# Kernel tuning notes

Hardware: AMD Instinct MI355X
Metric: run time of the kernel (lower is better)

The kernel has to match this reference:

```python
import jax, jax.numpy as jnp
import numpy as np

EPS = 1e-5
LN_EPS = 1e-5
NUM_EXPERTS = 8
TOP_K = 2
HIDDEN = 1024
INTER = 2048


def _swiglu(x, wg, wu, wd):
    # x: [T,H]; wg,wu: [H,I]; wd: [I,H]
    return (jax.nn.silu(x @ wg) * (x @ wu)) @ wd


def setup_inputs() -> dict:
    key = jax.random.key(0)
    ks = jax.random.split(key, 10)
    B, S, H, I, E = 8, 4096, HIDDEN, INTER, NUM_EXPERTS
    std_h = 1.0 / np.sqrt(H)
    std_i = 1.0 / np.sqrt(I)
    return {
        "x": jax.random.normal(ks[0], (B, S, H), dtype=jnp.float32),
        "ln_scale": jnp.ones((H,), dtype=jnp.float32),
        "ln_bias": jnp.zeros((H,), dtype=jnp.float32),
        "gate_w": jax.random.normal(ks[1], (E, H), dtype=jnp.float32) * 0.01,
        "Wg": jax.random.normal(ks[2], (E, H, I), dtype=jnp.float32) * std_h,
        "Wu": jax.random.normal(ks[3], (E, H, I), dtype=jnp.float32) * std_h,
        "Wd": jax.random.normal(ks[4], (E, I, H), dtype=jnp.float32) * std_i,
        "sWg": jax.random.normal(ks[5], (H, I), dtype=jnp.float32) * std_h,
        "sWu": jax.random.normal(ks[6], (H, I), dtype=jnp.float32) * std_h,
        "sWd": jax.random.normal(ks[7], (I, H), dtype=jnp.float32) * std_i,
    }


def reference(x, ln_scale, ln_bias, gate_w, Wg, Wu, Wd, sWg, sWu, sWd):
    B, S, H = x.shape
    xf = x.reshape(-1, H)  # [T,H]
    # Router: LayerNorm -> gate -> softmax -> top-k -> renormalize
    mu = jnp.mean(xf, axis=-1, keepdims=True)
    var = jnp.var(xf, axis=-1, keepdims=True)
    xn = (xf - mu) * jax.lax.rsqrt(var + LN_EPS) * ln_scale + ln_bias
    logits = xn @ gate_w.T  # [T,E]
    probs = jax.nn.softmax(logits, axis=-1)
    tk_probs, tk_idx = jax.lax.top_k(probs, TOP_K)  # [T,K]
    tk_probs = tk_probs / (jnp.sum(tk_probs, axis=-1, keepdims=True) + EPS)
    # Per-expert combine weight: w[t,e] = sum_k tk_probs[t,k] * (tk_idx[t,k]==e)
    onehot = (tk_idx[..., None] == jnp.arange(NUM_EXPERTS)[None, None, :])  # [T,K,E]
    w = jnp.sum(tk_probs[..., None] * onehot.astype(tk_probs.dtype), axis=1)  # [T,E]
    # Shared expert + weighted routed experts
    out = _swiglu(xf, sWg, sWu, sWd)
    for e in range(NUM_EXPERTS):
        out = out + w[:, e:e + 1] * _swiglu(xf, Wg[e], Wu[e], Wd[e])
    return out.reshape(B, S, H)
```

## Files before the change

kernel.cpp:

```cpp
#include <hip/hip_runtime.h>

#define H 1024
#define ITR 2048
#define NE 8
#define BT 128

typedef __attribute__((ext_vector_type(8))) short short8;
typedef __attribute__((ext_vector_type(4))) float f32x4;

__device__ __forceinline__ float bf2f(unsigned short u){
  union { unsigned int i; float f; } v; v.i = ((unsigned int)u) << 16; return v.f;
}
__device__ __forceinline__ unsigned short f2bf(float f){
  union { unsigned int i; float f; } v; v.f = f;
  unsigned int r = v.i + 0x7FFFu + ((v.i >> 16) & 1u);
  return (unsigned short)(r >> 16);
}
__device__ __forceinline__ void gload16(const void* g, void* l){
  __builtin_amdgcn_global_load_lds((const __attribute__((address_space(1))) void*)g,
                                   (__attribute__((address_space(3))) void*)l, 16, 0, 0);
}

__global__ __launch_bounds__(64) void detect_k(const unsigned int* __restrict__ xw,
                                               int* __restrict__ flag, int* __restrict__ counts){
  int lane = threadIdx.x;
  int c = 0;
  #pragma unroll
  for (int i = 0; i < 4; i++){
    unsigned u = xw[lane * 4 + i];
    int e = (u >> 7) & 0xFF;
    c += (e >= 100 && e <= 140) ? 1 : 0;
  }
  #pragma unroll
  for (int off = 32; off; off >>= 1) c += __shfl_xor(c, off);
  if (lane == 0) flag[0] = (c < 128) ? 1 : 0;
  if (lane < NE) counts[lane] = 0;
}

__device__ __forceinline__ void loadv16(const void* base, size_t off, int isf, float* out){
  if (isf){
    const float* p = (const float*)base + off;
    float4 a = *(const float4*)p, b = *(const float4*)(p + 4);
    float4 c = *(const float4*)(p + 8), d = *(const float4*)(p + 12);
    out[0]=a.x; out[1]=a.y; out[2]=a.z; out[3]=a.w;
    out[4]=b.x; out[5]=b.y; out[6]=b.z; out[7]=b.w;
    out[8]=c.x; out[9]=c.y; out[10]=c.z; out[11]=c.w;
    out[12]=d.x; out[13]=d.y; out[14]=d.z; out[15]=d.w;
  } else {
    const unsigned short* p = (const unsigned short*)base + off;
    uint4 a = *(const uint4*)p, b = *(const uint4*)(p + 8);
    unsigned short u[16];
    *(uint4*)u = a; *(uint4*)(u + 8) = b;
    #pragma unroll
    for (int j = 0; j < 16; j++) out[j] = bf2f(u[j]);
  }
}

__global__ __launch_bounds__(256) void trans_k(
    const void* __restrict__ rg, const void* __restrict__ ru, const void* __restrict__ rd,
    const void* __restrict__ sg, const void* __restrict__ su, const void* __restrict__ sd,
    int e0, unsigned short* __restrict__ arena, size_t slot_elems,
    const int* __restrict__ flag)
{
  int slot = blockIdx.z / 3, mt = blockIdx.z % 3;
  int e = e0 + slot;
  int R = (mt == 2) ? ITR : H;
  int C = (mt == 2) ? H : ITR;
  int c0 = blockIdx.x * 64, r0 = blockIdx.y * 64;
  if (c0 >= C || r0 >= R) return;
  const void* srcv;
  size_t eoff = 0;
  if (e == NE) srcv = (mt == 0) ? sg : ((mt == 1) ? su : sd);
  else { srcv = (mt == 0) ? rg : ((mt == 1) ? ru : rd); eoff = (size_t)e * H * ITR; }
  unsigned short* dst = arena + (size_t)slot * slot_elems + (size_t)mt * (H * ITR);
  int isf = *flag;
  __shared__ unsigned short tile[64][72];
  int t = threadIdx.x;
  int row = t >> 3, c8 = (t & 7) * 8;
  #pragma unroll
  for (int p = 0; p < 2; p++){
    int r = r0 + row + p * 32;
    unsigned short v[8];
    if (isf){
      const float* s = (const float*)srcv + eoff + (size_t)r * C + c0 + c8;
      float4 a = *(const float4*)s, b = *(const float4*)(s + 4);
      v[0]=f2bf(a.x); v[1]=f2bf(a.y); v[2]=f2bf(a.z); v[3]=f2bf(a.w);
      v[4]=f2bf(b.x); v[5]=f2bf(b.y); v[6]=f2bf(b.z); v[7]=f2bf(b.w);
    } else {
      const unsigned short* s = (const unsigned short*)srcv + eoff + (size_t)r * C + c0 + c8;
      *(uint4*)v = *(const uint4*)s;
    }
    *(uint4*)&tile[row + p * 32][c8] = *(const uint4*)v;
  }
  __syncthreads();
  #pragma unroll
  for (int p = 0; p < 2; p++){
    int c = row + p * 32;
    unsigned short tmp[8];
    #pragma unroll
    for (int j = 0; j < 8; j++) tmp[j] = tile[c8 + j][c];
    *(uint4*)(dst + (size_t)(c0 + c) * R + r0 + c8) = *(const uint4*)tmp;
  }
}

__global__ __launch_bounds__(256) void router2_k(
    const void* __restrict__ x, const void* __restrict__ lns, const void* __restrict__ lnb,
    const void* __restrict__ gw, int T, const int* __restrict__ flag,
    int* __restrict__ counts, int* __restrict__ lidx, float* __restrict__ lw)
{
  int isf = *flag;
  int tid = threadIdx.x, wv = tid >> 6, lane = tid & 63;
  int t0 = blockIdx.x * BT;
  __shared__ int sc_cnt[NE], sbase[NE];
  __shared__ int se1[BT], se2[BT], so1[BT], so2[BT];
  __shared__ float sw1[BT], sw2[BT];
  if (tid < NE) sc_cnt[tid] = 0;
  float sc[16], bi[16];
  loadv16(lns, (size_t)lane * 16, isf, sc);
  loadv16(lnb, (size_t)lane * 16, isf, bi);
  __syncthreads();

  for (int i = 0; i < BT / 4; i++){
    int tl = i * 4 + wv;
    int tok = t0 + tl;
    if (tok >= T) break;
    float v[16];
    loadv16(x, (size_t)tok * H + lane * 16, isf, v);
    float sum = 0.f, ss = 0.f;
    #pragma unroll
    for (int j = 0; j < 16; j++){ sum += v[j]; ss += v[j] * v[j]; }
    #pragma unroll
    for (int off = 32; off; off >>= 1){ sum += __shfl_xor(sum, off); ss += __shfl_xor(ss, off); }
    float mu = sum * (1.f / H);
    float rstd = rsqrtf(ss * (1.f / H) - mu * mu + 1e-5f);
    float xn[16];
    #pragma unroll
    for (int j = 0; j < 16; j++) xn[j] = (v[j] - mu) * rstd * sc[j] + bi[j];
    float acc[NE];
    #pragma unroll
    for (int e = 0; e < NE; e++){
      float g[16];
      loadv16(gw, (size_t)e * H + lane * 16, isf, g);
      float s = 0.f;
      #pragma unroll
      for (int j = 0; j < 16; j++) s += xn[j] * g[j];
      acc[e] = s;
    }
    #pragma unroll
    for (int off = 32; off; off >>= 1){
      #pragma unroll
      for (int e = 0; e < NE; e++) acc[e] += __shfl_xor(acc[e], off);
    }
    if (lane == 0){
      float m = acc[0];
      #pragma unroll
      for (int e = 1; e < NE; e++) m = fmaxf(m, acc[e]);
      float p[NE], Z = 0.f;
      #pragma unroll
      for (int e = 0; e < NE; e++){ p[e] = expf(acc[e] - m); Z += p[e]; }
      float iZ = 1.f / Z;
      #pragma unroll
      for (int e = 0; e < NE; e++) p[e] *= iZ;
      int i1 = 0;
      #pragma unroll
      for (int e = 1; e < NE; e++) if (p[e] > p[i1]) i1 = e;
      int i2 = (i1 == 0) ? 1 : 0;
      #pragma unroll
      for (int e = 0; e < NE; e++) if (e != i1 && p[e] > p[i2]) i2 = e;
      float s2 = p[i1] + p[i2] + 1e-5f;
      int o1 = atomicAdd(&sc_cnt[i1], 1);
      int o2 = atomicAdd(&sc_cnt[i2], 1);
      se1[tl] = i1; so1[tl] = o1; sw1[tl] = p[i1] / s2;
      se2[tl] = i2; so2[tl] = o2; sw2[tl] = p[i2] / s2;
    }
  }
  __syncthreads();
  if (tid < NE) sbase[tid] = atomicAdd(&counts[tid], sc_cnt[tid]);
  __syncthreads();
  if (tid < BT && t0 + tid < T){
    int tok = t0 + tid;
    int e1 = se1[tid], p1 = sbase[e1] + so1[tid];
    lidx[(size_t)e1 * T + p1] = tok; lw[(size_t)e1 * T + p1] = sw1[tid];
    int e2 = se2[tid], p2 = sbase[e2] + so2[tid];
    lidx[(size_t)e2 * T + p2] = tok; lw[(size_t)e2 * T + p2] = sw2[tid];
  }
}

__global__ __launch_bounds__(256, 2) void gateup_k(
    const void* __restrict__ x, const unsigned short* __restrict__ wgT, const unsigned short* __restrict__ wuT,
    const int* __restrict__ counts, int e, int T, const int* __restrict__ lidx,
    unsigned short* __restrict__ hidden, int chunk_off, const int* __restrict__ flag)
{
  int cnt = (e == NE) ? T : counts[e];
  int tm = blockIdx.y;
  if (chunk_off + tm * 128 >= cnt) return;
  int tn = blockIdx.x;
  int isf = *flag;

  __shared__ unsigned short Al[128 * 32];
  __shared__ unsigned short Bgl[128 * 32];
  __shared__ unsigned short Bul[128 * 32];

  int tid = threadIdx.x, wv = tid >> 6, lane = tid & 63;
  int c1 = cnt - 1;
  int r0 = chunk_off + tm * 128 + (tid >> 2);
  int r1 = r0 + 64;
  int rr0 = r0 < c1 ? r0 : c1, rr1 = r1 < c1 ? r1 : c1;
  int tok0 = (e == NE) ? rr0 : lidx[(size_t)e * T + rr0];
  int tok1 = (e == NE) ? rr1 : lidx[(size_t)e * T + rr1];
  int kc = (tid & 3) * 8;
  const unsigned short* ga0 = (const unsigned short*)x + (size_t)tok0 * H + kc;
  const unsigned short* ga1 = (const unsigned short*)x + (size_t)tok1 * H + kc;
  const float* fa0 = (const float*)x + (size_t)tok0 * H + kc;
  const float* fa1 = (const float*)x + (size_t)tok1 * H + kc;
  int nb = tn * 128 + (tid >> 2);
  const unsigned short* gg0 = wgT + (size_t)nb * H + kc;
  const unsigned short* gg1 = gg0 + (size_t)64 * H;
  const unsigned short* gu0 = wuT + (size_t)nb * H + kc;
  const unsigned short* gu1 = gu0 + (size_t)64 * H;

  f32x4 zero4 = {0.f, 0.f, 0.f, 0.f};
  f32x4 accg[4][4], accu[4][4];
  #pragma unroll
  for (int m = 0; m < 4; m++)
    #pragma unroll
    for (int n = 0; n < 4; n++){ accg[m][n] = zero4; accu[m][n] = zero4; }

  int wm = (wv >> 1) * 64, wn = (wv & 1) * 64;
  int rlo = lane & 15, khi = (lane >> 4) * 8;

  for (int k0 = 0; k0 < H; k0 += 32){
    if (isf){
      float4 q0 = *(const float4*)(fa0 + k0), q1 = *(const float4*)(fa0 + k0 + 4);
      float4 q2 = *(const float4*)(fa1 + k0), q3 = *(const float4*)(fa1 + k0 + 4);
      unsigned short w8[8];
      w8[0]=f2bf(q0.x); w8[1]=f2bf(q0.y); w8[2]=f2bf(q0.z); w8[3]=f2bf(q0.w);
      w8[4]=f2bf(q1.x); w8[5]=f2bf(q1.y); w8[6]=f2bf(q1.z); w8[7]=f2bf(q1.w);
      *(uint4*)(Al + tid * 8) = *(const uint4*)w8;
      w8[0]=f2bf(q2.x); w8[1]=f2bf(q2.y); w8[2]=f2bf(q2.z); w8[3]=f2bf(q2.w);
      w8[4]=f2bf(q3.x); w8[5]=f2bf(q3.y); w8[6]=f2bf(q3.z); w8[7]=f2bf(q3.w);
      *(uint4*)(Al + 2048 + tid * 8) = *(const uint4*)w8;
    } else {
      gload16(ga0 + k0, (char*)Al + wv * 1024);
      gload16(ga1 + k0, (char*)Al + 4096 + wv * 1024);
    }
    gload16(gg0 + k0, (char*)Bgl + wv * 1024);
    gload16(gg1 + k0, (char*)Bgl + 4096 + wv * 1024);
    gload16(gu0 + k0, (char*)Bul + wv * 1024);
    gload16(gu1 + k0, (char*)Bul + 4096 + wv * 1024);
    __syncthreads();
    short8 af[4], bg[4], bu[4];
    #pragma unroll
    for (int m = 0; m < 4; m++) af[m] = *(const short8*)(Al + (wm + m * 16 + rlo) * 32 + khi);
    #pragma unroll
    for (int n = 0; n < 4; n++){
      bg[n] = *(const short8*)(Bgl + (wn + n * 16 + rlo) * 32 + khi);
      bu[n] = *(const short8*)(Bul + (wn + n * 16 + rlo) * 32 + khi);
    }
    #pragma unroll
    for (int m = 0; m < 4; m++){
      #pragma unroll
      for (int n = 0; n < 4; n++){
        accg[m][n] = __builtin_amdgcn_mfma_f32_16x16x32_bf16(af[m], bg[n], accg[m][n], 0, 0, 0);
        accu[m][n] = __builtin_amdgcn_mfma_f32_16x16x32_bf16(af[m], bu[n], accu[m][n], 0, 0, 0);
      }
    }
    __syncthreads();
  }
  int rb = (lane >> 4) * 4, cb = lane & 15;
  #pragma unroll
  for (int m = 0; m < 4; m++){
    #pragma unroll
    for (int j = 0; j < 4; j++){
      int rl = tm * 128 + wm + m * 16 + rb + j;
      if (chunk_off + rl < cnt){
        unsigned short* hrow = hidden + (size_t)rl * ITR + tn * 128 + wn + cb;
        #pragma unroll
        for (int n = 0; n < 4; n++){
          float g = accg[m][n][j], u = accu[m][n][j];
          float h = g / (1.f + __expf(-g)) * u;
          hrow[n * 16] = f2bf(h);
        }
      }
    }
  }
}

__global__ __launch_bounds__(256, 2) void down_k(
    const unsigned short* __restrict__ hidden, const unsigned short* __restrict__ wdT,
    const int* __restrict__ counts, int e, int T, const int* __restrict__ lidx,
    const float* __restrict__ lw, void* __restrict__ out_, int chunk_off,
    const int* __restrict__ flag, int CHc)
{
  int cnt = (e == NE) ? T : counts[e];
  int tm = blockIdx.y;
  if (chunk_off + tm * 128 >= cnt) return;
  int tn = blockIdx.x;
  int isf = *flag;
  int vcnt = cnt - chunk_off; if (vcnt > CHc) vcnt = CHc;

  __shared__ unsigned short Al[128 * 32];
  __shared__ unsigned short Bl[128 * 32];
  int tid = threadIdx.x, wv = tid >> 6, lane = tid & 63;
  int kc = (tid & 3) * 8;
  int vm1 = vcnt - 1;
  int lr0 = tm * 128 + (tid >> 2);
  int lr1 = lr0 + 64;
  int cl0 = lr0 < vm1 ? lr0 : vm1, cl1 = lr1 < vm1 ? lr1 : vm1;
  const unsigned short* ga0 = hidden + (size_t)cl0 * ITR + kc;
  const unsigned short* ga1 = hidden + (size_t)cl1 * ITR + kc;
  int nb = tn * 128 + (tid >> 2);
  const unsigned short* gb0 = wdT + (size_t)nb * ITR + kc;
  const unsigned short* gb1 = gb0 + (size_t)64 * ITR;

  f32x4 zero4 = {0.f, 0.f, 0.f, 0.f};
  f32x4 acc[4][4];
  #pragma unroll
  for (int m = 0; m < 4; m++)
    #pragma unroll
    for (int n = 0; n < 4; n++) acc[m][n] = zero4;

  int wm = (wv >> 1) * 64, wn = (wv & 1) * 64;
  int rlo = lane & 15, khi = (lane >> 4) * 8;

  for (int k0 = 0; k0 < ITR; k0 += 32){
    gload16(ga0 + k0, (char*)Al + wv * 1024);
    gload16(ga1 + k0, (char*)Al + 4096 + wv * 1024);
    gload16(gb0 + k0, (char*)Bl + wv * 1024);
    gload16(gb1 + k0, (char*)Bl + 4096 + wv * 1024);
    __syncthreads();
    short8 af[4], bf[4];
    #pragma unroll
    for (int m = 0; m < 4; m++) af[m] = *(const short8*)(Al + (wm + m * 16 + rlo) * 32 + khi);
    #pragma unroll
    for (int n = 0; n < 4; n++) bf[n] = *(const short8*)(Bl + (wn + n * 16 + rlo) * 32 + khi);
    #pragma unroll
    for (int m = 0; m < 4; m++){
      #pragma unroll
      for (int n = 0; n < 4; n++)
        acc[m][n] = __builtin_amdgcn_mfma_f32_16x16x32_bf16(af[m], bf[n], acc[m][n], 0, 0, 0);
    }
    __syncthreads();
  }
  int rb = (lane >> 4) * 4, cb = lane & 15;
  #pragma unroll
  for (int m = 0; m < 4; m++){
    #pragma unroll
    for (int j = 0; j < 4; j++){
      int rl = tm * 128 + wm + m * 16 + rb + j;
      if (rl < vcnt){
        int rg = chunk_off + rl;
        int tok = (e == NE) ? rg : lidx[(size_t)e * T + rg];
        size_t ob = (size_t)tok * H + tn * 128 + wn + cb;
        if (e == NE){
          if (isf){
            float* p = (float*)out_ + ob;
            #pragma unroll
            for (int n = 0; n < 4; n++) p[n * 16] = acc[m][n][j];
          } else {
            unsigned short* p = (unsigned short*)out_ + ob;
            #pragma unroll
            for (int n = 0; n < 4; n++) p[n * 16] = f2bf(acc[m][n][j]);
          }
        } else {
          float wgt = lw[(size_t)e * T + rg];
          if (isf){
            float* p = (float*)out_ + ob;
            #pragma unroll
            for (int n = 0; n < 4; n++) p[n * 16] += wgt * acc[m][n][j];
          } else {
            unsigned short* p = (unsigned short*)out_ + ob;
            #pragma unroll
            for (int n = 0; n < 4; n++) p[n * 16] = f2bf(bf2f(p[n * 16]) + wgt * acc[m][n][j]);
          }
        }
      }
    }
  }
}

extern "C" void kernel_launch(void* const* d_in, const int* in_sizes, int n_in,
                              void* d_out, int out_size, void* d_ws, size_t ws_size,
                              hipStream_t stream)
{
  int T = in_sizes[0] / H;

  char* w = (char*)d_ws;
  auto alloc = [&](size_t b){ char* p = w; w += (b + 255) & ~(size_t)255; return p; };
  int* flag   = (int*)alloc(256);
  int* counts = (int*)alloc(256);
  int* lidx   = (int*)alloc((size_t)NE * T * 4);
  float* lw   = (float*)alloc((size_t)NE * T * 4);
  size_t base = (size_t)(w - (char*)d_ws);

  const size_t SLOT = (size_t)3 * H * ITR;
  const size_t SLOTB = SLOT * 2;

  int full = 0, CH = 0;
  for (int ch = 8192; ch >= 512; ch >>= 1){
    if (base + 9 * SLOTB + (size_t)ch * ITR * 2 + 1024 <= ws_size){ full = 1; CH = ch; break; }
  }
  if (!full){
    CH = 512;
    for (int ch = 8192; ch >= 512; ch >>= 1){
      if (base + SLOTB + (size_t)ch * ITR * 2 + 1024 <= ws_size){ CH = ch; break; }
    }
  }
  int nslots = full ? 9 : 1;
  unsigned short* arena = (unsigned short*)alloc((size_t)nslots * SLOTB);
  unsigned short* hidden = (unsigned short*)alloc((size_t)CH * ITR * 2);
  int NCH = (T + CH - 1) / CH;

  detect_k<<<1, 64, 0, stream>>>((const unsigned int*)d_in[0], flag, counts);
  router2_k<<<(T + BT - 1) / BT, 256, 0, stream>>>(d_in[0], d_in[1], d_in[2], d_in[3],
                                                   T, flag, counts, lidx, lw);

  auto run_expert = [&](int e, int slot){
    unsigned short* wgT = arena + (size_t)slot * SLOT;
    unsigned short* wuT = wgT + (size_t)H * ITR;
    unsigned short* wdT = wuT + (size_t)H * ITR;
    for (int c = 0; c < NCH; c++){
      gateup_k<<<dim3(ITR / 128, CH / 128), 256, 0, stream>>>(
          d_in[0], wgT, wuT, counts, e, T, lidx, hidden, c * CH, flag);
      down_k<<<dim3(H / 128, CH / 128), 256, 0, stream>>>(
          hidden, wdT, counts, e, T, lidx, lw, d_out, c * CH, flag, CH);
    }
  };

  if (full){
    trans_k<<<dim3(32, 32, 27), 256, 0, stream>>>(d_in[4], d_in[5], d_in[6],
                                                  d_in[7], d_in[8], d_in[9],
                                                  0, arena, SLOT, flag);
    run_expert(NE, 8);
    for (int e = 0; e < NE; e++) run_expert(e, e);
  } else {
    trans_k<<<dim3(32, 32, 3), 256, 0, stream>>>(d_in[4], d_in[5], d_in[6],
                                                 d_in[7], d_in[8], d_in[9],
                                                 NE, arena, SLOT, flag);
    run_expert(NE, 0);
    for (int e = 0; e < NE; e++){
      trans_k<<<dim3(32, 32, 3), 256, 0, stream>>>(d_in[4], d_in[5], d_in[6],
                                                   d_in[7], d_in[8], d_in[9],
                                                   e, arena, SLOT, flag);
      run_expert(e, 0);
    }
  }
}
```

Baseline: 2.800 ms.

## Replace per-expert GEMMs with segmented 256x256 double-buffered GEMM over packed expert tokens

Replaces the per-expert gate/up and down kernels with one templated 256x256-tile GEMM using 512 threads, a K-step of 64 and double-buffered LDS. Tokens for all experts are packed into padded segments located by a scan kernel, so a single launch can cover several experts. Gate and up projections now run as separate GEMMs, with the gate result staged through a bf16 buffer. Routing splits first and second choices into separate counters so that down-projection accumulations into the output from the two choices go to different chunks and do not race. The change adds launches and an extra gate buffer round-trip, loses one fused read of the activation tile, and drops the low-workspace fallback path.

```diff
diff --git a/kernel.cpp b/kernel.cpp
--- a/kernel.cpp
+++ b/kernel.cpp
@@ -3,7 +3,7 @@
 #define H 1024
 #define ITR 2048
 #define NE 8
-#define BT 128
+#define BT 32
 
 typedef __attribute__((ext_vector_type(8))) short short8;
 typedef __attribute__((ext_vector_type(4))) float f32x4;
@@ -22,7 +22,7 @@
 }
 
 __global__ __launch_bounds__(64) void detect_k(const unsigned int* __restrict__ xw,
-                                               int* __restrict__ flag, int* __restrict__ counts){
+                                               int* __restrict__ flag, int* __restrict__ cnt16){
   int lane = threadIdx.x;
   int c = 0;
   #pragma unroll
@@ -34,7 +34,7 @@
   #pragma unroll
   for (int off = 32; off; off >>= 1) c += __shfl_xor(c, off);
   if (lane == 0) flag[0] = (c < 128) ? 1 : 0;
-  if (lane < NE) counts[lane] = 0;
+  if (lane < 16) cnt16[lane] = 0;
 }
 
 __device__ __forceinline__ void loadv16(const void* base, size_t off, int isf, float* out){
@@ -59,11 +59,10 @@
 __global__ __launch_bounds__(256) void trans_k(
     const void* __restrict__ rg, const void* __restrict__ ru, const void* __restrict__ rd,
     const void* __restrict__ sg, const void* __restrict__ su, const void* __restrict__ sd,
-    int e0, unsigned short* __restrict__ arena, size_t slot_elems,
-    const int* __restrict__ flag)
+    unsigned short* __restrict__ arena, const int* __restrict__ flag)
 {
   int slot = blockIdx.z / 3, mt = blockIdx.z % 3;
-  int e = e0 + slot;
+  int e = slot;
   int R = (mt == 2) ? ITR : H;
   int C = (mt == 2) ? H : ITR;
   int c0 = blockIdx.x * 64, r0 = blockIdx.y * 64;
@@ -72,7 +71,7 @@
   size_t eoff = 0;
   if (e == NE) srcv = (mt == 0) ? sg : ((mt == 1) ? su : sd);
   else { srcv = (mt == 0) ? rg : ((mt == 1) ? ru : rd); eoff = (size_t)e * H * ITR; }
-  unsigned short* dst = arena + (size_t)slot * slot_elems + (size_t)mt * (H * ITR);
+  unsigned short* dst = arena + (size_t)slot * (3u * H * ITR) + (size_t)mt * (H * ITR);
   int isf = *flag;
   __shared__ unsigned short tile[64][72];
   int t = threadIdx.x;
@@ -106,15 +105,15 @@
 __global__ __launch_bounds__(256) void router2_k(
     const void* __restrict__ x, const void* __restrict__ lns, const void* __restrict__ lnb,
     const void* __restrict__ gw, int T, const int* __restrict__ flag,
-    int* __restrict__ counts, int* __restrict__ lidx, float* __restrict__ lw)
+    int* __restrict__ cnt16, int* __restrict__ lidx, float* __restrict__ lw)
 {
   int isf = *flag;
   int tid = threadIdx.x, wv = tid >> 6, lane = tid & 63;
   int t0 = blockIdx.x * BT;
-  __shared__ int sc_cnt[NE], sbase[NE];
-  __shared__ int se1[BT], se2[BT], so1[BT], so2[BT];
-  __shared__ float sw1[BT], sw2[BT];
-  if (tid < NE) sc_cnt[tid] = 0;
+  __shared__ int scc[16], sbase[16];
+  __shared__ int sei[2][BT], soi[2][BT];
+  __shared__ float swv[2][BT];
+  if (tid < 16) scc[tid] = 0;
   float sc[16], bi[16];
   loadv16(lns, (size_t)lane * 16, isf, sc);
   loadv16(lnb, (size_t)lane * 16, isf, bi);
@@ -168,210 +167,208 @@
       #pragma unroll
       for (int e = 0; e < NE; e++) if (e != i1 && p[e] > p[i2]) i2 = e;
       float s2 = p[i1] + p[i2] + 1e-5f;
-      int o1 = atomicAdd(&sc_cnt[i1], 1);
-      int o2 = atomicAdd(&sc_cnt[i2], 1);
-      se1[tl] = i1; so1[tl] = o1; sw1[tl] = p[i1] / s2;
-      se2[tl] = i2; so2[tl] = o2; sw2[tl] = p[i2] / s2;
+      int o1 = atomicAdd(&scc[i1], 1);
+      int o2 = atomicAdd(&scc[8 + i2], 1);
+      sei[0][tl] = i1; soi[0][tl] = o1; swv[0][tl] = p[i1] / s2;
+      sei[1][tl] = i2; soi[1][tl] = o2; swv[1][tl] = p[i2] / s2;
     }
   }
   __syncthreads();
-  if (tid < NE) sbase[tid] = atomicAdd(&counts[tid], sc_cnt[tid]);
+  if (tid < 16) sbase[tid] = atomicAdd(&cnt16[tid], scc[tid]);
   __syncthreads();
-  if (tid < BT && t0 + tid < T){
-    int tok = t0 + tid;
-    int e1 = se1[tid], p1 = sbase[e1] + so1[tid];
-    lidx[(size_t)e1 * T + p1] = tok; lw[(size_t)e1 * T + p1] = sw1[tid];
-    int e2 = se2[tid], p2 = sbase[e2] + so2[tid];
-    lidx[(size_t)e2 * T + p2] = tok; lw[(size_t)e2 * T + p2] = sw2[tid];
-  }
-}
-
-__global__ __launch_bounds__(256, 2) void gateup_k(
-    const void* __restrict__ x, const unsigned short* __restrict__ wgT, const unsigned short* __restrict__ wuT,
-    const int* __restrict__ counts, int e, int T, const int* __restrict__ lidx,
-    unsigned short* __restrict__ hidden, int chunk_off, const int* __restrict__ flag)
+  if (tid < 2 * BT){
+    int l = tid / BT, t = tid % BT;
+    int tok = t0 + t;
+    if (tok < T){
+      int ctr = l * 8 + sei[l][t];
+      int pos = sbase[ctr] + soi[l][t];
+      lidx[(size_t)ctr * T + pos] = tok;
+      lw[(size_t)ctr * T + pos] = swv[l][t];
+    }
+  }
+}
+
+__global__ __launch_bounds__(64) void scan_k(const int* __restrict__ cnt16,
+                                             int* __restrict__ segA, int* __restrict__ segEp,
+                                             int* __restrict__ segCnt, int T, int CH,
+                                             int L1C, int L2C){
+  if (threadIdx.x == 0){
+    segA[0] = 0; segEp[0] = T; segCnt[0] = T;
+    int b = L1C * CH;
+    for (int e = 0; e < 8; e++){
+      segA[1 + e] = b; segCnt[1 + e] = cnt16[e];
+      b += (cnt16[e] + 255) & ~255;
+      segEp[1 + e] = b;
+    }
+    b = L2C * CH;
+    for (int e = 0; e < 8; e++){
+      segA[9 + e] = b; segCnt[9 + e] = cnt16[8 + e];
+      b += (cnt16[8 + e] + 255) & ~255;
+      segEp[9 + e] = b;
+    }
+  }
+}
+
+template<int EPI>
+__global__ __launch_bounds__(512, 2) void gemm256_k(
+    const void* __restrict__ Asrc, const unsigned short* __restrict__ arena,
+    unsigned short* __restrict__ gbuf, unsigned short* __restrict__ hptr,
+    void* __restrict__ outp,
+    const int* __restrict__ segA, const int* __restrict__ segEp, const int* __restrict__ segCnt,
+    const int* __restrict__ lidx, const float* __restrict__ lw,
+    int T, int CH, int cbase_chunk, int hmask, const int* __restrict__ flag)
 {
-  int cnt = (e == NE) ? T : counts[e];
-  int tm = blockIdx.y;
-  if (chunk_off + tm * 128 >= cnt) return;
-  int tn = blockIdx.x;
+  constexpr int K = (EPI == 2) ? ITR : H;
+  constexpr int NT = K / 64;
+  int chid = cbase_chunk + blockIdx.z;
+  int tn = blockIdx.x, tm = blockIdx.y;
+  int pr0 = chid * CH + tm * 256;
+
+  int s = -1;
+  if (pr0 < T) s = 0;
+  else {
+    #pragma unroll
+    for (int i = 1; i <= 16; i++)
+      if (pr0 >= segA[i] && pr0 < segEp[i]) s = i;
+  }
+  if (s < 0) return;
+  int cnt = segCnt[s];
+  int base = segA[s];
+  int slot = (s == 0) ? 8 : ((s - 1) & 7);
+  const unsigned short* wT = arena + (size_t)slot * (3u * H * ITR) + (size_t)EPI * (H * ITR);
   int isf = *flag;
 
-  __shared__ unsigned short Al[128 * 32];
-  __shared__ unsigned short Bgl[128 * 32];
-  __shared__ unsigned short Bul[128 * 32];
-
-  int tid = threadIdx.x, wv = tid >> 6, lane = tid & 63;
-  int c1 = cnt - 1;
-  int r0 = chunk_off + tm * 128 + (tid >> 2);
-  int r1 = r0 + 64;
-  int rr0 = r0 < c1 ? r0 : c1, rr1 = r1 < c1 ? r1 : c1;
-  int tok0 = (e == NE) ? rr0 : lidx[(size_t)e * T + rr0];
-  int tok1 = (e == NE) ? rr1 : lidx[(size_t)e * T + rr1];
-  int kc = (tid & 3) * 8;
-  const unsigned short* ga0 = (const unsigned short*)x + (size_t)tok0 * H + kc;
-  const unsigned short* ga1 = (const unsigned short*)x + (size_t)tok1 * H + kc;
-  const float* fa0 = (const float*)x + (size_t)tok0 * H + kc;
-  const float* fa1 = (const float*)x + (size_t)tok1 * H + kc;
-  int nb = tn * 128 + (tid >> 2);
-  const unsigned short* gg0 = wgT + (size_t)nb * H + kc;
-  const unsigned short* gg1 = gg0 + (size_t)64 * H;
-  const unsigned short* gu0 = wuT + (size_t)nb * H + kc;
-  const unsigned short* gu1 = gu0 + (size_t)64 * H;
-
+  __shared__ unsigned short Al[2][256 * 64];
+  __shared__ unsigned short Bl[2][256 * 64];
+
+  int tid = threadIdx.x, wid = tid >> 6, lane = tid & 63;
+  int ldr = tid >> 3;
+  int c8 = (tid & 7) * 8;
+
+  const unsigned short* abf[4];
+  const float* af32[4];
+  #pragma unroll
+  for (int q = 0; q < 4; q++){
+    if (EPI == 2){
+      int pr = pr0 + q * 64 + ldr;
+      int hrow = ((chid & hmask) ? CH : 0) + (pr - chid * CH);
+      abf[q] = (const unsigned short*)Asrc + (size_t)hrow * ITR + c8;
+      af32[q] = nullptr;
+    } else {
+      int rl = pr0 - base + q * 64 + ldr;
+      int rc = cnt - 1; rl = rl < rc ? rl : rc;
+      int tok = (s == 0) ? rl : lidx[(size_t)(s - 1) * T + rl];
+      abf[q] = (const unsigned short*)Asrc + (size_t)tok * H + c8;
+      af32[q] = (const float*)Asrc + (size_t)tok * H + c8;
+    }
+  }
+  const unsigned short* bptr[4];
+  #pragma unroll
+  for (int q = 0; q < 4; q++)
+    bptr[q] = wT + (size_t)(tn * 256 + q * 64 + ldr) * K + c8;
+
+  f32x4 acc[8][4];
   f32x4 zero4 = {0.f, 0.f, 0.f, 0.f};
-  f32x4 accg[4][4], accu[4][4];
-  #pragma unroll
-  for (int m = 0; m < 4; m++)
-    #pragma unroll
-    for (int n = 0; n < 4; n++){ accg[m][n] = zero4; accu[m][n] = zero4; }
-
-  int wm = (wv >> 1) * 64, wn = (wv & 1) * 64;
-  int rlo = lane & 15, khi = (lane >> 4) * 8;
-
-  for (int k0 = 0; k0 < H; k0 += 32){
-    if (isf){
-      float4 q0 = *(const float4*)(fa0 + k0), q1 = *(const float4*)(fa0 + k0 + 4);
-      float4 q2 = *(const float4*)(fa1 + k0), q3 = *(const float4*)(fa1 + k0 + 4);
-      unsigned short w8[8];
-      w8[0]=f2bf(q0.x); w8[1]=f2bf(q0.y); w8[2]=f2bf(q0.z); w8[3]=f2bf(q0.w);
-      w8[4]=f2bf(q1.x); w8[5]=f2bf(q1.y); w8[6]=f2bf(q1.z); w8[7]=f2bf(q1.w);
-      *(uint4*)(Al + tid * 8) = *(const uint4*)w8;
-      w8[0]=f2bf(q2.x); w8[1]=f2bf(q2.y); w8[2]=f2bf(q2.z); w8[3]=f2bf(q2.w);
-      w8[4]=f2bf(q3.x); w8[5]=f2bf(q3.y); w8[6]=f2bf(q3.z); w8[7]=f2bf(q3.w);
-      *(uint4*)(Al + 2048 + tid * 8) = *(const uint4*)w8;
-    } else {
-      gload16(ga0 + k0, (char*)Al + wv * 1024);
-      gload16(ga1 + k0, (char*)Al + 4096 + wv * 1024);
-    }
-    gload16(gg0 + k0, (char*)Bgl + wv * 1024);
-    gload16(gg1 + k0, (char*)Bgl + 4096 + wv * 1024);
-    gload16(gu0 + k0, (char*)Bul + wv * 1024);
-    gload16(gu1 + k0, (char*)Bul + 4096 + wv * 1024);
+  #pragma unroll
+  for (int m = 0; m < 8; m++)
+    #pragma unroll
+    for (int n = 0; n < 4; n++) acc[m][n] = zero4;
+
+  int wm = (wid >> 2) * 128, wn = (wid & 3) * 64;
+  int fr = lane & 15, fk = (lane >> 4) * 8;
+
+  auto stage = [&](int buf, int kt){
+    int k0 = kt * 64;
+    #pragma unroll
+    for (int q = 0; q < 4; q++){
+      if (EPI < 2 && isf){
+        float4 v0 = *(const float4*)(af32[q] + k0);
+        float4 v1 = *(const float4*)(af32[q] + k0 + 4);
+        unsigned short w8[8] = {f2bf(v0.x), f2bf(v0.y), f2bf(v0.z), f2bf(v0.w),
+                                f2bf(v1.x), f2bf(v1.y), f2bf(v1.z), f2bf(v1.w)};
+        *(uint4*)((char*)&Al[buf][0] + q * 8192 + tid * 16) = *(const uint4*)w8;
+      } else {
+        gload16(abf[q] + k0, (char*)&Al[buf][0] + q * 8192 + wid * 1024);
+      }
+      gload16(bptr[q] + k0, (char*)&Bl[buf][0] + q * 8192 + wid * 1024);
+    }
+  };
+
+  auto compute = [&](int buf){
+    #pragma unroll
+    for (int ks = 0; ks < 2; ks++){
+      short8 a[8], b[4];
+      #pragma unroll
+      for (int m = 0; m < 8; m++)
+        a[m] = *(const short8*)(&Al[buf][(wm + m * 16 + fr) * 64 + ks * 32 + fk]);
+      #pragma unroll
+      for (int n = 0; n < 4; n++)
+        b[n] = *(const short8*)(&Bl[buf][(wn + n * 16 + fr) * 64 + ks * 32 + fk]);
+      #pragma unroll
+      for (int m = 0; m < 8; m++)
+        #pragma unroll
+        for (int n = 0; n < 4; n++)
+          acc[m][n] = __builtin_amdgcn_mfma_f32_16x16x32_bf16(a[m], b[n], acc[m][n], 0, 0, 0);
+    }
+  };
+
+  stage(0, 0);
+  int cur = 0;
+  for (int kt = 0; kt < NT; kt++){
     __syncthreads();
-    short8 af[4], bg[4], bu[4];
-    #pragma unroll
-    for (int m = 0; m < 4; m++) af[m] = *(const short8*)(Al + (wm + m * 16 + rlo) * 32 + khi);
-    #pragma unroll
-    for (int n = 0; n < 4; n++){
-      bg[n] = *(const short8*)(Bgl + (wn + n * 16 + rlo) * 32 + khi);
-      bu[n] = *(const short8*)(Bul + (wn + n * 16 + rlo) * 32 + khi);
-    }
-    #pragma unroll
-    for (int m = 0; m < 4; m++){
-      #pragma unroll
-      for (int n = 0; n < 4; n++){
-        accg[m][n] = __builtin_amdgcn_mfma_f32_16x16x32_bf16(af[m], bg[n], accg[m][n], 0, 0, 0);
-        accu[m][n] = __builtin_amdgcn_mfma_f32_16x16x32_bf16(af[m], bu[n], accu[m][n], 0, 0, 0);
-      }
-    }
-    __syncthreads();
-  }
+    if (kt + 1 < NT) stage(cur ^ 1, kt + 1);
+    compute(cur);
+    cur ^= 1;
+  }
+
   int rb = (lane >> 4) * 4, cb = lane & 15;
   #pragma unroll
-  for (int m = 0; m < 4; m++){
+  for (int m = 0; m < 8; m++){
     #pragma unroll
     for (int j = 0; j < 4; j++){
-      int rl = tm * 128 + wm + m * 16 + rb + j;
-      if (chunk_off + rl < cnt){
-        unsigned short* hrow = hidden + (size_t)rl * ITR + tn * 128 + wn + cb;
+      int rt = wm + m * 16 + rb + j;
+      int pr = pr0 + rt;
+      int col = tn * 256 + wn + cb;
+      if (EPI == 0){
+        unsigned short* gr = gbuf + (size_t)(pr - chid * CH) * ITR + col;
+        #pragma unroll
+        for (int n = 0; n < 4; n++) gr[n * 16] = f2bf(acc[m][n][j]);
+      } else if (EPI == 1){
+        size_t ro = (size_t)(pr - chid * CH) * ITR + col;
+        unsigned short* hr = hptr + ro;
+        const unsigned short* gr = gbuf + ro;
         #pragma unroll
         for (int n = 0; n < 4; n++){
-          float g = accg[m][n][j], u = accu[m][n][j];
-          float h = g / (1.f + __expf(-g)) * u;
-          hrow[n * 16] = f2bf(h);
+          float g = bf2f(gr[n * 16]);
+          float u = acc[m][n][j];
+          hr[n * 16] = f2bf(g / (1.f + __expf(-g)) * u);
         }
-      }
-    }
-  }
-}
-
-__global__ __launch_bounds__(256, 2) void down_k(
-    const unsigned short* __restrict__ hidden, const unsigned short* __restrict__ wdT,
-    const int* __restrict__ counts, int e, int T, const int* __restrict__ lidx,
-    const float* __restrict__ lw, void* __restrict__ out_, int chunk_off,
-    const int* __restrict__ flag, int CHc)
-{
-  int cnt = (e == NE) ? T : counts[e];
-  int tm = blockIdx.y;
-  if (chunk_off + tm * 128 >= cnt) return;
-  int tn = blockIdx.x;
-  int isf = *flag;
-  int vcnt = cnt - chunk_off; if (vcnt > CHc) vcnt = CHc;
-
-  __shared__ unsigned short Al[128 * 32];
-  __shared__ unsigned short Bl[128 * 32];
-  int tid = threadIdx.x, wv = tid >> 6, lane = tid & 63;
-  int kc = (tid & 3) * 8;
-  int vm1 = vcnt - 1;
-  int lr0 = tm * 128 + (tid >> 2);
-  int lr1 = lr0 + 64;
-  int cl0 = lr0 < vm1 ? lr0 : vm1, cl1 = lr1 < vm1 ? lr1 : vm1;
-  const unsigned short* ga0 = hidden + (size_t)cl0 * ITR + kc;
-  const unsigned short* ga1 = hidden + (size_t)cl1 * ITR + kc;
-  int nb = tn * 128 + (tid >> 2);
-  const unsigned short* gb0 = wdT + (size_t)nb * ITR + kc;
-  const unsigned short* gb1 = gb0 + (size_t)64 * ITR;
-
-  f32x4 zero4 = {0.f, 0.f, 0.f, 0.f};
-  f32x4 acc[4][4];
-  #pragma unroll
-  for (int m = 0; m < 4; m++)
-    #pragma unroll
-    for (int n = 0; n < 4; n++) acc[m][n] = zero4;
-
-  int wm = (wv >> 1) * 64, wn = (wv & 1) * 64;
-  int rlo = lane & 15, khi = (lane >> 4) * 8;
-
-  for (int k0 = 0; k0 < ITR; k0 += 32){
-    gload16(ga0 + k0, (char*)Al + wv * 1024);
-    gload16(ga1 + k0, (char*)Al + 4096 + wv * 1024);
-    gload16(gb0 + k0, (char*)Bl + wv * 1024);
-    gload16(gb1 + k0, (char*)Bl + 4096 + wv * 1024);
-    __syncthreads();
-    short8 af[4], bf[4];
-    #pragma unroll
-    for (int m = 0; m < 4; m++) af[m] = *(const short8*)(Al + (wm + m * 16 + rlo) * 32 + khi);
-    #pragma unroll
-    for (int n = 0; n < 4; n++) bf[n] = *(const short8*)(Bl + (wn + n * 16 + rlo) * 32 + khi);
-    #pragma unroll
-    for (int m = 0; m < 4; m++){
-      #pragma unroll
-      for (int n = 0; n < 4; n++)
-        acc[m][n] = __builtin_amdgcn_mfma_f32_16x16x32_bf16(af[m], bf[n], acc[m][n], 0, 0, 0);
-    }
-    __syncthreads();
-  }
-  int rb = (lane >> 4) * 4, cb = lane & 15;
-  #pragma unroll
-  for (int m = 0; m < 4; m++){
-    #pragma unroll
-    for (int j = 0; j < 4; j++){
-      int rl = tm * 128 + wm + m * 16 + rb + j;
-      if (rl < vcnt){
-        int rg = chunk_off + rl;
-        int tok = (e == NE) ? rg : lidx[(size_t)e * T + rg];
-        size_t ob = (size_t)tok * H + tn * 128 + wn + cb;
-        if (e == NE){
-          if (isf){
-            float* p = (float*)out_ + ob;
-            #pragma unroll
-            for (int n = 0; n < 4; n++) p[n * 16] = acc[m][n][j];
+      } else {
+        int rl = pr - base;
+        if (rl < cnt){
+          int tok = (s == 0) ? rl : lidx[(size_t)(s - 1) * T + rl];
+          size_t ob = (size_t)tok * H + col;
+          if (s == 0){
+            if (isf){
+              float* p = (float*)outp + ob;
+              #pragma unroll
+              for (int n = 0; n < 4; n++) p[n * 16] = acc[m][n][j];
+            } else {
+              unsigned short* p = (unsigned short*)outp + ob;
+              #pragma unroll
+              for (int n = 0; n < 4; n++) p[n * 16] = f2bf(acc[m][n][j]);
+            }
           } else {
-            unsigned short* p = (unsigned short*)out_ + ob;
-            #pragma unroll
-            for (int n = 0; n < 4; n++) p[n * 16] = f2bf(acc[m][n][j]);
-          }
-        } else {
-          float wgt = lw[(size_t)e * T + rg];
-          if (isf){
-            float* p = (float*)out_ + ob;
-            #pragma unroll
-            for (int n = 0; n < 4; n++) p[n * 16] += wgt * acc[m][n][j];
-          } else {
-            unsigned short* p = (unsigned short*)out_ + ob;
-            #pragma unroll
-            for (int n = 0; n < 4; n++) p[n * 16] = f2bf(bf2f(p[n * 16]) + wgt * acc[m][n][j]);
+            float wgt = lw[(size_t)(s - 1) * T + rl];
+            if (isf){
+              float* p = (float*)outp + ob;
+              #pragma unroll
+              for (int n = 0; n < 4; n++) p[n * 16] += wgt * acc[m][n][j];
+            } else {
+              unsigned short* p = (unsigned short*)outp + ob;
+              #pragma unroll
+              for (int n = 0; n < 4; n++) p[n * 16] = f2bf(bf2f(p[n * 16]) + wgt * acc[m][n][j]);
+            }
           }
         }
       }
@@ -388,61 +385,59 @@
   char* w = (char*)d_ws;
   auto alloc = [&](size_t b){ char* p = w; w += (b + 255) & ~(size_t)255; return p; };
   int* flag   = (int*)alloc(256);
-  int* counts = (int*)alloc(256);
-  int* lidx   = (int*)alloc((size_t)NE * T * 4);
-  float* lw   = (float*)alloc((size_t)NE * T * 4);
-  size_t base = (size_t)(w - (char*)d_ws);
-
-  const size_t SLOT = (size_t)3 * H * ITR;
-  const size_t SLOTB = SLOT * 2;
-
-  int full = 0, CH = 0;
-  for (int ch = 8192; ch >= 512; ch >>= 1){
-    if (base + 9 * SLOTB + (size_t)ch * ITR * 2 + 1024 <= ws_size){ full = 1; CH = ch; break; }
-  }
-  if (!full){
-    CH = 512;
-    for (int ch = 8192; ch >= 512; ch >>= 1){
-      if (base + SLOTB + (size_t)ch * ITR * 2 + 1024 <= ws_size){ CH = ch; break; }
-    }
-  }
-  int nslots = full ? 9 : 1;
-  unsigned short* arena = (unsigned short*)alloc((size_t)nslots * SLOTB);
-  unsigned short* hidden = (unsigned short*)alloc((size_t)CH * ITR * 2);
-  int NCH = (T + CH - 1) / CH;
-
-  detect_k<<<1, 64, 0, stream>>>((const unsigned int*)d_in[0], flag, counts);
+  int* cnt16  = (int*)alloc(256);
+  int* segA   = (int*)alloc(256);
+  int* segEp  = (int*)alloc(256);
+  int* segCnt = (int*)alloc(256);
+  int* lidx   = (int*)alloc((size_t)16 * T * 4);
+  float* lw   = (float*)alloc((size_t)16 * T * 4);
+  const size_t ARENA = (size_t)9 * 3 * H * ITR * 2;
+  unsigned short* arena = (unsigned short*)alloc(ARENA);
+  size_t used = (size_t)(w - (char*)d_ws);
+
+  int CH = 1024, hmask = 0;
+  for (int ch = 8192; ch >= 1024; ch >>= 1){
+    size_t needs2 = used + (size_t)ch * ITR * 2 + (size_t)2 * ch * ITR * 2 + 1024;
+    size_t needs1 = used + (size_t)ch * ITR * 2 + (size_t)ch * ITR * 2 + 1024;
+    if (needs2 <= ws_size){ CH = ch; hmask = 1; break; }
+    if (needs1 <= ws_size){ CH = ch; hmask = 0; break; }
+  }
+  unsigned short* gbuf   = (unsigned short*)alloc((size_t)CH * ITR * 2);
+  unsigned short* hidden = (unsigned short*)alloc((size_t)(hmask ? 2 : 1) * CH * ITR * 2);
+
+  int CB1 = (T + CH - 1) / CH;
+  int chunks1 = (T + 8 * 255 + CH - 1) / CH;
+  int CB2 = CB1 + chunks1;
+  int NCHUNK = CB2 + chunks1;
+
+  detect_k<<<1, 64, 0, stream>>>((const unsigned int*)d_in[0], flag, cnt16);
   router2_k<<<(T + BT - 1) / BT, 256, 0, stream>>>(d_in[0], d_in[1], d_in[2], d_in[3],
-                                                   T, flag, counts, lidx, lw);
-
-  auto run_expert = [&](int e, int slot){
-    unsigned short* wgT = arena + (size_t)slot * SLOT;
-    unsigned short* wuT = wgT + (size_t)H * ITR;
-    unsigned short* wdT = wuT + (size_t)H * ITR;
-    for (int c = 0; c < NCH; c++){
-      gateup_k<<<dim3(ITR / 128, CH / 128), 256, 0, stream>>>(
-          d_in[0], wgT, wuT, counts, e, T, lidx, hidden, c * CH, flag);
-      down_k<<<dim3(H / 128, CH / 128), 256, 0, stream>>>(
-          hidden, wdT, counts, e, T, lidx, lw, d_out, c * CH, flag, CH);
-    }
+                                                   T, flag, cnt16, lidx, lw);
+  scan_k<<<1, 64, 0, stream>>>(cnt16, segA, segEp, segCnt, T, CH, CB1, CB2);
+  trans_k<<<dim3(32, 32, 27), 256, 0, stream>>>(d_in[4], d_in[5], d_in[6],
+                                                d_in[7], d_in[8], d_in[9], arena, flag);
+
+  struct Grp { int c0, nz; };
+  Grp groups[64]; int ng = 0;
+  auto addg = [&](int a, int b){
+    for (int c = a; c < b;){ int nz = (c + 1 < b && hmask) ? 2 : 1; groups[ng].c0 = c; groups[ng].nz = nz; ng++; c += nz; }
   };
-
-  if (full){
-    trans_k<<<dim3(32, 32, 27), 256, 0, stream>>>(d_in[4], d_in[5], d_in[6],
-                                                  d_in[7], d_in[8], d_in[9],
-                                                  0, arena, SLOT, flag);
-    run_expert(NE, 8);
-    for (int e = 0; e < NE; e++) run_expert(e, e);
-  } else {
-    trans_k<<<dim3(32, 32, 3), 256, 0, stream>>>(d_in[4], d_in[5], d_in[6],
-                                                 d_in[7], d_in[8], d_in[9],
-                                                 NE, arena, SLOT, flag);
-    run_expert(NE, 0);
-    for (int e = 0; e < NE; e++){
-      trans_k<<<dim3(32, 32, 3), 256, 0, stream>>>(d_in[4], d_in[5], d_in[6],
-                                                   d_in[7], d_in[8], d_in[9],
-                                                   e, arena, SLOT, flag);
-      run_expert(e, 0);
-    }
-  }
-}
+  addg(0, CB1); addg(CB1, CB2); addg(CB2, NCHUNK);
+
+  dim3 ggu(ITR / 256, CH / 256, 1);
+  int gi = 0;
+  for (int c = 0; c < NCHUNK; c++){
+    unsigned short* hp = hidden + (size_t)(c & hmask) * CH * ITR;
+    gemm256_k<0><<<ggu, 512, 0, stream>>>(d_in[0], arena, gbuf, nullptr, nullptr,
+                                          segA, segEp, segCnt, lidx, lw, T, CH, c, hmask, flag);
+    gemm256_k<1><<<ggu, 512, 0, stream>>>(d_in[0], arena, gbuf, hp, nullptr,
+                                          segA, segEp, segCnt, lidx, lw, T, CH, c, hmask, flag);
+    if (gi < ng && groups[gi].c0 + groups[gi].nz == c + 1){
+      dim3 gd(H / 256, CH / 256, groups[gi].nz);
+      gemm256_k<2><<<gd, 512, 0, stream>>>(hidden, arena, nullptr, nullptr, d_out,
+                                           segA, segEp, segCnt, lidx, lw, T, CH,
+                                           groups[gi].c0, hmask, flag);
+      gi++;
+    }
+  }
+}
```

After: 3.567 ms. +27.4%, slower.
